# Optimization experiments

Measured on AMD Instinct MI355X. Metric: run time of the kernel, lower is better.

Reference implementation:

```python
import jax, jax.numpy as jnp
import numpy as np

N_NODES = 50000
N_EDGES = 800000
IN_DIM = 128
HID = 64
OUT_DIM = 128
N_GRAPHS = 256


def setup_inputs() -> dict:
    key = jax.random.key(0)
    ks = jax.random.split(key, 8)
    x = jax.random.normal(ks[0], (N_NODES, IN_DIM), dtype=jnp.float32)
    edge_index = jax.random.randint(ks[1], (2, N_EDGES), 0, N_NODES, dtype=jnp.int64)
    batch = jnp.sort(jax.random.randint(ks[2], (N_NODES,), 0, N_GRAPHS, dtype=jnp.int64))
    # Glorot-ish init for GCN weights, zero bias (PyG default bias=True)
    W1 = jax.random.normal(ks[3], (IN_DIM, HID), dtype=jnp.float32) / np.sqrt(IN_DIM)
    b1 = jnp.zeros((HID,), dtype=jnp.float32)
    W2 = jax.random.normal(ks[4], (HID, HID), dtype=jnp.float32) / np.sqrt(HID)
    b2 = jnp.zeros((HID,), dtype=jnp.float32)
    W3 = jax.random.normal(ks[5], (HID, OUT_DIM), dtype=jnp.float32) / np.sqrt(HID)
    b3 = jnp.zeros((OUT_DIM,), dtype=jnp.float32)
    return {"x": x, "edge_index": edge_index, "batch": batch, "num_graphs": N_GRAPHS,
            "W1": W1, "b1": b1, "W2": W2, "b2": b2, "W3": W3, "b3": b3}


def _gcn_norm(edge_index, n_nodes):
    # PyG GCNConv default: add self-loops, symmetric D^{-1/2}(A+I)D^{-1/2} norm.
    loops = jnp.arange(n_nodes, dtype=edge_index.dtype)
    src = jnp.concatenate([edge_index[0], loops])  # [E + N]
    dst = jnp.concatenate([edge_index[1], loops])
    deg = jax.ops.segment_sum(jnp.ones_like(dst, dtype=jnp.float32), dst,
                              num_segments=n_nodes)
    dinv = jnp.where(deg > 0, jax.lax.rsqrt(jnp.maximum(deg, 1.0)), 0.0)
    norm = dinv[src] * dinv[dst]  # [E + N]
    return src, dst, norm


def _gcn_conv(x, W, b, src, dst, norm, n_nodes):
    h = x @ W                                  # [N, F_out] dense GEMM
    msg = h[src] * norm[:, None]               # gather + scale  [E+N, F_out]
    agg = jax.ops.segment_sum(msg, dst, num_segments=n_nodes)
    return agg + b


def reference(x, edge_index, batch, num_graphs, W1, b1, W2, b2, W3, b3):
    n_nodes = x.shape[0]
    src, dst, norm = _gcn_norm(edge_index, n_nodes)
    h = jax.nn.gelu(_gcn_conv(x, W1, b1, src, dst, norm, n_nodes))
    h = jax.nn.gelu(_gcn_conv(h, W2, b2, src, dst, norm, n_nodes))
    h = _gcn_conv(h, W3, b3, src, dst, norm, n_nodes)
    # global_mean_pool over batch segment ids
    sums = jax.ops.segment_sum(h, batch, num_segments=num_graphs)
    counts = jax.ops.segment_sum(jnp.ones((n_nodes,), dtype=h.dtype), batch,
                                 num_segments=num_graphs)
    return sums / jnp.maximum(counts, 1.0)[:, None]
```

## Files before the change

### kernel.cpp

```cpp
#include <hip/hip_runtime.h>
#include <hip/hip_fp16.h>
#include <math.h>

#define N_NODES   50000
#define N_EDGES   800000
#define IN_DIM    128
#define HID       64
#define OUT_DIM   128
#define N_GRAPHS  256
#define MAX_DEG   64
#define PARTS     8
#define PSIZE     (N_NODES / PARTS)
#define EPB       4096

typedef _Float16 half8 __attribute__((ext_vector_type(8)));
typedef float floatx4 __attribute__((ext_vector_type(4)));


__global__ __launch_bounds__(256) void k_build(const int* __restrict__ src,
                                               const int* __restrict__ dst,
                                               int* __restrict__ deg, int* __restrict__ col) {
    int p     = blockIdx.x & (PARTS - 1);
    int chunk = blockIdx.x >> 3;
    int base  = chunk * EPB;
    int lo = p * PSIZE, hi = lo + PSIZE;
#pragma unroll
    for (int j = 0; j < EPB / 256; j++) {
        int e = base + j * 256 + threadIdx.x;
        if (e < N_EDGES) {
            int d = dst[e];
            if (d >= lo && d < hi) {
                int pos = atomicAdd(&deg[d], 1);
                if (pos < MAX_DEG) col[d * MAX_DEG + pos] = src[e];
            }
        }
    }
}

__global__ void k_dinv(const int* __restrict__ deg, float* __restrict__ dinv) {
    int n = blockIdx.x * blockDim.x + threadIdx.x;
    if (n < N_NODES) dinv[n] = rsqrtf((float)(deg[n] + 1));
}

__global__ void k_pack(const float* __restrict__ W, __half* __restrict__ Wt, int K) {
    int idx = blockIdx.x * blockDim.x + threadIdx.x;
    int total = (K / 8) * 64;
    if (idx < total) {
        int g = idx >> 6, n = idx & 63;
#pragma unroll
        for (int i = 0; i < 8; i++)
            Wt[idx * 8 + i] = __float2half(W[(8 * g + i) * 64 + n]);
    }
}


__global__ __launch_bounds__(256) void k_mfma1(const float* __restrict__ A,
                                               const float* __restrict__ dinv,
                                               const __half* __restrict__ Bp,
                                               __half* __restrict__ C) {
    constexpr int K = IN_DIM, S = K / 32;
    int wv   = threadIdx.x >> 6;
    int lane = threadIdx.x & 63;
    int quad = lane >> 4, l15 = lane & 15;
    int row0 = blockIdx.x * 64 + wv * 16;
    if (row0 >= N_NODES) return;

    half8 bf[S][4];
#pragma unroll
    for (int s = 0; s < S; s++)
#pragma unroll
        for (int j = 0; j < 4; j++)
            bf[s][j] = *(const half8*)(Bp + ((size_t)((4 * s + quad) * 64 + 16 * j + l15)) * 8);

    floatx4 acc[4];
#pragma unroll
    for (int j = 0; j < 4; j++) acc[j] = 0.f;

    int arow = row0 + l15;
    float dv = dinv[arow];
#pragma unroll
    for (int s = 0; s < S; s++) {
        float4 xa = *(const float4*)(A + (size_t)arow * K + 32 * s + quad * 8);
        float4 xb = *(const float4*)(A + (size_t)arow * K + 32 * s + quad * 8 + 4);
        half8 af;
        af[0] = (_Float16)(xa.x * dv); af[1] = (_Float16)(xa.y * dv);
        af[2] = (_Float16)(xa.z * dv); af[3] = (_Float16)(xa.w * dv);
        af[4] = (_Float16)(xb.x * dv); af[5] = (_Float16)(xb.y * dv);
        af[6] = (_Float16)(xb.z * dv); af[7] = (_Float16)(xb.w * dv);
#pragma unroll
        for (int j = 0; j < 4; j++)
            acc[j] = __builtin_amdgcn_mfma_f32_16x16x32_f16(af, bf[s][j], acc[j], 0, 0, 0);
    }
#pragma unroll
    for (int j = 0; j < 4; j++)
#pragma unroll
        for (int r = 0; r < 4; r++)
            C[(size_t)(row0 + quad * 4 + r) * 64 + 16 * j + l15] = __float2half(acc[j][r]);
}


__global__ __launch_bounds__(256) void k_mfma2(const __half* __restrict__ A,
                                               const __half* __restrict__ Bp,
                                               __half* __restrict__ C) {
    constexpr int K = HID, S = K / 32;
    int wv   = threadIdx.x >> 6;
    int lane = threadIdx.x & 63;
    int quad = lane >> 4, l15 = lane & 15;
    int row0 = blockIdx.x * 64 + wv * 16;
    if (row0 >= N_NODES) return;

    half8 bf[S][4];
#pragma unroll
    for (int s = 0; s < S; s++)
#pragma unroll
        for (int j = 0; j < 4; j++)
            bf[s][j] = *(const half8*)(Bp + ((size_t)((4 * s + quad) * 64 + 16 * j + l15)) * 8);

    floatx4 acc[4];
#pragma unroll
    for (int j = 0; j < 4; j++) acc[j] = 0.f;

    int arow = row0 + l15;
#pragma unroll
    for (int s = 0; s < S; s++) {
        half8 af = *(const half8*)(A + (size_t)arow * K + 32 * s + quad * 8);
#pragma unroll
        for (int j = 0; j < 4; j++)
            acc[j] = __builtin_amdgcn_mfma_f32_16x16x32_f16(af, bf[s][j], acc[j], 0, 0, 0);
    }
#pragma unroll
    for (int j = 0; j < 4; j++)
#pragma unroll
        for (int r = 0; r < 4; r++)
            C[(size_t)(row0 + quad * 4 + r) * 64 + 16 * j + l15] = __float2half(acc[j][r]);
}


__device__ __forceinline__ void addv(float4& acc, uint2 v) {
    __half2 va = *(__half2*)&v.x, vb = *(__half2*)&v.y;
    acc.x += __low2float(va); acc.y += __high2float(va);
    acc.z += __low2float(vb); acc.w += __high2float(vb);
}

__global__ __launch_bounds__(256) void k_agg(const __half* __restrict__ T,
                                             const int* __restrict__ col,
                                             const int* __restrict__ indeg,
                                             const float* __restrict__ dinv,
                                             const float* __restrict__ b,
                                             __half* __restrict__ OUT, int mode) {
    int lane = threadIdx.x & 63;
    int wv   = threadIdx.x >> 6;
    int q = lane >> 4, t = lane & 15;
    int d = (blockIdx.x * 4 + wv) * 4 + q;
    int dg = indeg[d]; if (dg > MAX_DEG) dg = MAX_DEG;
    int m1 = max(dg, __shfl_xor(dg, 16));
    int mx = max(m1, __shfl_xor(m1, 32));

    uint2 u = *(const uint2*)(T + (size_t)d * HID + 4 * t);
    float4 acc = make_float4(0.f, 0.f, 0.f, 0.f);
    addv(acc, u);

    for (int base = 0; base < mx; base += 16) {
        int c = (base + t < dg) ? col[d * MAX_DEG + base + t] : 0;
        int lim = mx - base; if (lim > 16) lim = 16;
        int i = 0;
        for (; i + 4 <= lim; i += 4) {
            int s0 = __shfl(c, q * 16 + i,     64);
            int s1 = __shfl(c, q * 16 + i + 1, 64);
            int s2 = __shfl(c, q * 16 + i + 2, 64);
            int s3 = __shfl(c, q * 16 + i + 3, 64);
            uint2 v0 = *(const uint2*)(T + (size_t)s0 * HID + 4 * t);
            uint2 v1 = *(const uint2*)(T + (size_t)s1 * HID + 4 * t);
            uint2 v2 = *(const uint2*)(T + (size_t)s2 * HID + 4 * t);
            uint2 v3 = *(const uint2*)(T + (size_t)s3 * HID + 4 * t);
            if (base + i     < dg) addv(acc, v0);
            if (base + i + 1 < dg) addv(acc, v1);
            if (base + i + 2 < dg) addv(acc, v2);
            if (base + i + 3 < dg) addv(acc, v3);
        }
        for (; i < lim; i++) {
            int s = __shfl(c, q * 16 + i, 64);
            uint2 v = *(const uint2*)(T + (size_t)s * HID + 4 * t);
            if (base + i < dg) addv(acc, v);
        }
    }

    float dv = dinv[d];
    float o[4] = {acc.x * dv, acc.y * dv, acc.z * dv, acc.w * dv};
    if (mode == 0) {
#pragma unroll
        for (int j = 0; j < 4; j++) {
            float v = o[j] + b[4 * t + j];
            float u2 = 0.7978845608028654f * (v + 0.044715f * v * v * v);
            o[j] = 0.5f * v * (1.0f + tanhf(u2)) * dv;
        }
    }
    __half2 s0 = __floats2half2_rn(o[0], o[1]);
    __half2 s1 = __floats2half2_rn(o[2], o[3]);
    uint2 st; st.x = *(unsigned*)&s0; st.y = *(unsigned*)&s1;
    *(uint2*)(OUT + (size_t)d * HID + 4 * t) = st;
}


__global__ __launch_bounds__(256) void k_pool_out(const __half* __restrict__ A,
                                                  const int* __restrict__ batch,
                                                  const float* __restrict__ W3,
                                                  const float* __restrict__ b3,
                                                  float* __restrict__ out) {
    int g = blockIdx.x;
    int lo = 0, hi = N_NODES;
    while (lo < hi) { int m = (lo + hi) >> 1; if (batch[m] < g) lo = m + 1; else hi = m; }
    int lo2 = lo, hi2 = N_NODES;
    while (lo2 < hi2) { int m = (lo2 + hi2) >> 1; if (batch[m] < g + 1) lo2 = m + 1; else hi2 = m; }
    int start = lo, end = lo2;

    int lane = threadIdx.x & 63;
    int wave = threadIdx.x >> 6;
    float acc = 0.f;
    for (int n = start + wave; n < end; n += 4)
        acc += __half2float(A[(size_t)n * HID + lane]);

    __shared__ float part[4][HID];
    __shared__ float pooled[HID];
    part[wave][lane] = acc;
    __syncthreads();
    if (threadIdx.x < HID)
        pooled[threadIdx.x] = part[0][threadIdx.x] + part[1][threadIdx.x] +
                              part[2][threadIdx.x] + part[3][threadIdx.x];
    __syncthreads();

    if (threadIdx.x < OUT_DIM) {
        float cntf = (float)(end - start);
        float inv = 1.0f / fmaxf(cntf, 1.0f);
        float s = 0.f;
#pragma unroll
        for (int k = 0; k < HID; k++) s += pooled[k] * W3[k * OUT_DIM + threadIdx.x];
        out[g * OUT_DIM + threadIdx.x] = (s + cntf * b3[threadIdx.x]) * inv;
    }
}


extern "C" void kernel_launch(void* const* d_in, const int* in_sizes, int n_in,
                              void* d_out, int out_size, void* d_ws, size_t ws_size,
                              hipStream_t stream) {
    const float* x     = (const float*)d_in[0];
    const int*   ei    = (const int*)d_in[1];
    const int*   batch = (const int*)d_in[2];
    const float* W1    = (const float*)d_in[4];
    const float* b1    = (const float*)d_in[5];
    const float* W2    = (const float*)d_in[6];
    const float* b2    = (const float*)d_in[7];
    const float* W3    = (const float*)d_in[8];
    const float* b3    = (const float*)d_in[9];
    float* out = (float*)d_out;

    const int* esrc = ei;
    const int* edst = ei + N_EDGES;

    int*    deg  = (int*)d_ws;
    float*  dinv = (float*)(deg + N_NODES);
    int*    col  = (int*)(dinv + N_NODES);
    __half* t    = (__half*)(col + (size_t)N_NODES * MAX_DEG);
    __half* p    = t + (size_t)N_NODES * HID;
    __half* Wt1  = p + (size_t)N_NODES * HID;
    __half* Wt2  = Wt1 + IN_DIM * HID;

    hipMemsetAsync(deg, 0, (size_t)N_NODES * 4, stream);

    const int CHUNKS = (N_EDGES + EPB - 1) / EPB;
    k_build<<<CHUNKS * PARTS, 256, 0, stream>>>(esrc, edst, deg, col);
    k_dinv<<<(N_NODES + 255) / 256, 256, 0, stream>>>(deg, dinv);
    k_pack<<<((IN_DIM / 8) * 64 + 255) / 256, 256, 0, stream>>>(W1, Wt1, IN_DIM);
    k_pack<<<((HID / 8) * 64 + 255) / 256, 256, 0, stream>>>(W2, Wt2, HID);

    const int GB = (N_NODES + 63) / 64;
    const int AB = N_NODES / 16;

    k_mfma1<<<GB, 256, 0, stream>>>(x, dinv, Wt1, t);
    k_agg<<<AB, 256, 0, stream>>>(t, col, deg, dinv, b1, p, 0);
    k_mfma2<<<GB, 256, 0, stream>>>(p, Wt2, t);
    k_agg<<<AB, 256, 0, stream>>>(t, col, deg, dinv, b2, p, 0);
    k_agg<<<AB, 256, 0, stream>>>(p, col, deg, dinv, b3, t, 1);
    k_pool_out<<<N_GRAPHS, 256, 0, stream>>>(t, batch, W3, b3, out);
}
```

Measured before the change: 221.1 us.

## Stage neighbor lists in LDS and widen aggregation gathers to 16 bytes

The aggregation kernel now assigns 8 lanes per destination node, each gathering 16-byte chunks, and processes 32 nodes per block. Each block first copies all 64 column slots per node into shared memory, which replaces the per-wave shuffles and the loop over the wave's maximum degree. Separately, the dinv and two weight-packing kernels are merged into one launch. The trade-off is that every block reads the full padded column array regardless of actual degree, and lanes within a wave now diverge on per-node degree.

```diff
diff --git a/kernel.cpp b/kernel.cpp
--- a/kernel.cpp
+++ b/kernel.cpp
@@ -12,6 +12,7 @@
 #define PARTS     8
 #define PSIZE     (N_NODES / PARTS)
 #define EPB       4096
+#define AGG_NPB   32
 
 typedef _Float16 half8 __attribute__((ext_vector_type(8)));
 typedef float floatx4 __attribute__((ext_vector_type(4)));
@@ -37,19 +38,28 @@
     }
 }
 
-__global__ void k_dinv(const int* __restrict__ deg, float* __restrict__ dinv) {
-    int n = blockIdx.x * blockDim.x + threadIdx.x;
-    if (n < N_NODES) dinv[n] = rsqrtf((float)(deg[n] + 1));
-}
-
-__global__ void k_pack(const float* __restrict__ W, __half* __restrict__ Wt, int K) {
-    int idx = blockIdx.x * blockDim.x + threadIdx.x;
-    int total = (K / 8) * 64;
-    if (idx < total) {
+__global__ __launch_bounds__(256) void k_prep(const int* __restrict__ deg,
+                                              float* __restrict__ dinv,
+                                              const float* __restrict__ W1, __half* __restrict__ Wt1,
+                                              const float* __restrict__ W2, __half* __restrict__ Wt2) {
+    int blk = blockIdx.x;
+    if (blk < 196) {
+        int n = blk * 256 + threadIdx.x;
+        if (n < N_NODES) dinv[n] = rsqrtf((float)(deg[n] + 1));
+    } else if (blk < 200) {
+        int idx = (blk - 196) * 256 + threadIdx.x;
         int g = idx >> 6, n = idx & 63;
 #pragma unroll
         for (int i = 0; i < 8; i++)
-            Wt[idx * 8 + i] = __float2half(W[(8 * g + i) * 64 + n]);
+            Wt1[idx * 8 + i] = __float2half(W1[(8 * g + i) * 64 + n]);
+    } else {
+        int idx = (blk - 200) * 256 + threadIdx.x;
+        if (idx < 512) {
+            int g = idx >> 6, n = idx & 63;
+#pragma unroll
+            for (int i = 0; i < 8; i++)
+                Wt2[idx * 8 + i] = __float2half(W2[(8 * g + i) * 64 + n]);
+        }
     }
 }
 
@@ -136,10 +146,13 @@
 }
 
 
-__device__ __forceinline__ void addv(float4& acc, uint2 v) {
-    __half2 va = *(__half2*)&v.x, vb = *(__half2*)&v.y;
-    acc.x += __low2float(va); acc.y += __high2float(va);
-    acc.z += __low2float(vb); acc.w += __high2float(vb);
+__device__ __forceinline__ void add8(float* acc, uint4 v) {
+    const __half2* h = (const __half2*)&v;
+#pragma unroll
+    for (int j = 0; j < 4; j++) {
+        acc[2 * j]     += __low2float(h[j]);
+        acc[2 * j + 1] += __high2float(h[j]);
+    }
 }
 
 __global__ __launch_bounds__(256) void k_agg(const __half* __restrict__ T,
@@ -148,57 +161,61 @@
                                              const float* __restrict__ dinv,
                                              const float* __restrict__ b,
                                              __half* __restrict__ OUT, int mode) {
+    __shared__ int cols[AGG_NPB][MAX_DEG + 1];
+    int base = blockIdx.x * AGG_NPB;
+
+    for (int idx = threadIdx.x; idx < AGG_NPB * MAX_DEG; idx += 256) {
+        int r = idx >> 6, j = idx & 63;
+        int g = base + r;
+        if (g < N_NODES) cols[r][j] = col[g * MAX_DEG + j];
+    }
+    __syncthreads();
+
     int lane = threadIdx.x & 63;
     int wv   = threadIdx.x >> 6;
-    int q = lane >> 4, t = lane & 15;
-    int d = (blockIdx.x * 4 + wv) * 4 + q;
+    int q = lane >> 3, t = lane & 7;
+    int local = wv * 8 + q;
+    int d = base + local;
+    if (d >= N_NODES) return;
+
     int dg = indeg[d]; if (dg > MAX_DEG) dg = MAX_DEG;
-    int m1 = max(dg, __shfl_xor(dg, 16));
-    int mx = max(m1, __shfl_xor(m1, 32));
-
-    uint2 u = *(const uint2*)(T + (size_t)d * HID + 4 * t);
-    float4 acc = make_float4(0.f, 0.f, 0.f, 0.f);
-    addv(acc, u);
-
-    for (int base = 0; base < mx; base += 16) {
-        int c = (base + t < dg) ? col[d * MAX_DEG + base + t] : 0;
-        int lim = mx - base; if (lim > 16) lim = 16;
-        int i = 0;
-        for (; i + 4 <= lim; i += 4) {
-            int s0 = __shfl(c, q * 16 + i,     64);
-            int s1 = __shfl(c, q * 16 + i + 1, 64);
-            int s2 = __shfl(c, q * 16 + i + 2, 64);
-            int s3 = __shfl(c, q * 16 + i + 3, 64);
-            uint2 v0 = *(const uint2*)(T + (size_t)s0 * HID + 4 * t);
-            uint2 v1 = *(const uint2*)(T + (size_t)s1 * HID + 4 * t);
-            uint2 v2 = *(const uint2*)(T + (size_t)s2 * HID + 4 * t);
-            uint2 v3 = *(const uint2*)(T + (size_t)s3 * HID + 4 * t);
-            if (base + i     < dg) addv(acc, v0);
-            if (base + i + 1 < dg) addv(acc, v1);
-            if (base + i + 2 < dg) addv(acc, v2);
-            if (base + i + 3 < dg) addv(acc, v3);
-        }
-        for (; i < lim; i++) {
-            int s = __shfl(c, q * 16 + i, 64);
-            uint2 v = *(const uint2*)(T + (size_t)s * HID + 4 * t);
-            if (base + i < dg) addv(acc, v);
-        }
+
+    float acc[8];
+#pragma unroll
+    for (int j = 0; j < 8; j++) acc[j] = 0.f;
+    add8(acc, *(const uint4*)(T + (size_t)d * HID + t * 8));
+
+    const int* cl = cols[local];
+    int i = 0;
+    for (; i + 4 <= dg; i += 4) {
+        int s0 = cl[i], s1 = cl[i + 1], s2 = cl[i + 2], s3 = cl[i + 3];
+        uint4 v0 = *(const uint4*)(T + (size_t)s0 * HID + t * 8);
+        uint4 v1 = *(const uint4*)(T + (size_t)s1 * HID + t * 8);
+        uint4 v2 = *(const uint4*)(T + (size_t)s2 * HID + t * 8);
+        uint4 v3 = *(const uint4*)(T + (size_t)s3 * HID + t * 8);
+        add8(acc, v0); add8(acc, v1); add8(acc, v2); add8(acc, v3);
+    }
+    for (; i < dg; i++) {
+        int s = cl[i];
+        add8(acc, *(const uint4*)(T + (size_t)s * HID + t * 8));
     }
 
     float dv = dinv[d];
-    float o[4] = {acc.x * dv, acc.y * dv, acc.z * dv, acc.w * dv};
+    float o[8];
+#pragma unroll
+    for (int j = 0; j < 8; j++) o[j] = acc[j] * dv;
     if (mode == 0) {
 #pragma unroll
-        for (int j = 0; j < 4; j++) {
-            float v = o[j] + b[4 * t + j];
+        for (int j = 0; j < 8; j++) {
+            float v = o[j] + b[t * 8 + j];
             float u2 = 0.7978845608028654f * (v + 0.044715f * v * v * v);
             o[j] = 0.5f * v * (1.0f + tanhf(u2)) * dv;
         }
     }
-    __half2 s0 = __floats2half2_rn(o[0], o[1]);
-    __half2 s1 = __floats2half2_rn(o[2], o[3]);
-    uint2 st; st.x = *(unsigned*)&s0; st.y = *(unsigned*)&s1;
-    *(uint2*)(OUT + (size_t)d * HID + 4 * t) = st;
+    __half2 hh[4];
+#pragma unroll
+    for (int j = 0; j < 4; j++) hh[j] = __floats2half2_rn(o[2 * j], o[2 * j + 1]);
+    *(uint4*)(OUT + (size_t)d * HID + t * 8) = *(uint4*)hh;
 }
 
 
@@ -269,12 +286,10 @@
 
     const int CHUNKS = (N_EDGES + EPB - 1) / EPB;
     k_build<<<CHUNKS * PARTS, 256, 0, stream>>>(esrc, edst, deg, col);
-    k_dinv<<<(N_NODES + 255) / 256, 256, 0, stream>>>(deg, dinv);
-    k_pack<<<((IN_DIM / 8) * 64 + 255) / 256, 256, 0, stream>>>(W1, Wt1, IN_DIM);
-    k_pack<<<((HID / 8) * 64 + 255) / 256, 256, 0, stream>>>(W2, Wt2, HID);
+    k_prep<<<202, 256, 0, stream>>>(deg, dinv, W1, Wt1, W2, Wt2);
 
     const int GB = (N_NODES + 63) / 64;
-    const int AB = N_NODES / 16;
+    const int AB = (N_NODES + AGG_NPB - 1) / AGG_NPB;
 
     k_mfma1<<<GB, 256, 0, stream>>>(x, dinv, Wt1, t);
     k_agg<<<AB, 256, 0, stream>>>(t, col, deg, dinv, b1, p, 0);
```

Result: faster. 214.2 us (-3.1%).
